# Kernel optimization log

Measured on AMD Instinct MI355X. Metric: run time of the kernel, lower is better.

Reference implementation:

```python
import jax, jax.numpy as jnp
import numpy as np

B, T, V = 512, 200, 2048
E, H, I, A = 20, 100, 64, 32  # embedding, hidden, intermediate, actions


def setup_inputs() -> dict:
    key = jax.random.key(0)
    ks = jax.random.split(key, 12)
    batch = jax.random.uniform(ks[0], (B, T, V), dtype=jnp.float32)
    lengths = jax.random.randint(ks[1], (B,), 1, T + 1)
    s = 0.05
    W_emb = jax.random.normal(ks[2], (E, V), dtype=jnp.float32) * s
    b_emb = jnp.zeros((E,), jnp.float32)
    W_ih = jax.random.normal(ks[3], (4 * H, E), dtype=jnp.float32) * s
    W_hh = jax.random.normal(ks[4], (4 * H, H), dtype=jnp.float32) * s
    b_ih = jnp.zeros((4 * H,), jnp.float32)
    # torch init sets forget-gate bias (second quarter) to 1.0 in bias_hh
    b_hh = jnp.zeros((4 * H,), jnp.float32).at[H:2 * H].set(1.0)
    W1 = jax.random.normal(ks[5], (I, H), dtype=jnp.float32) * s
    b1 = jnp.zeros((I,), jnp.float32)
    W2 = jax.random.normal(ks[6], (A, I), dtype=jnp.float32) * s
    b2 = jnp.zeros((A,), jnp.float32)
    h0 = jnp.zeros((B, H), jnp.float32)
    c0 = jnp.zeros((B, H), jnp.float32)
    return {"batch": batch, "lengths": lengths, "W_emb": W_emb, "b_emb": b_emb,
            "W_ih": W_ih, "W_hh": W_hh, "b_ih": b_ih, "b_hh": b_hh,
            "W1": W1, "b1": b1, "W2": W2, "b2": b2, "h0": h0, "c0": c0}


def reference(batch, lengths, W_emb, b_emb, W_ih, W_hh, b_ih, b_hh,
              W1, b1, W2, b2, h0, c0):
    # Embedding via Linear: [B,T,V] @ [V,E] -> [B,T,E]
    emb = jnp.einsum('btv,ev->bte', batch, W_emb) + b_emb
    # Precompute input contribution to all gates: [B,T,4H]
    xg = jnp.einsum('bte,ge->btg', emb, W_ih) + b_ih + b_hh

    def step(carry, xg_t):
        h, c = carry
        gates = xg_t + h @ W_hh.T  # [B,4H]
        i, f, g, o = jnp.split(gates, 4, axis=-1)  # torch gate order i,f,g,o
        c = jax.nn.sigmoid(f) * c + jax.nn.sigmoid(i) * jnp.tanh(g)
        h = jax.nn.sigmoid(o) * jnp.tanh(c)
        return (h, c), h

    _, ys = jax.lax.scan(step, (h0, c0), jnp.swapaxes(xg, 0, 1))  # ys: [T,B,H]
    nb = batch.shape[0]
    h_final = ys[lengths - 1, jnp.arange(nb)]  # [B,H] output at last valid step
    inter = jax.nn.relu(h_final @ W1.T + b1)
    actions = inter @ W2.T + b2
    return actions
```

## Files before the change

### kernel.cpp

```cpp
#include <hip/hip_runtime.h>

#define BB 512
#define TT 200
#define VV 2048
#define EE 20
#define HH 100
#define G4 400
#define II 64
#define AA 32

typedef _Float16 half8 __attribute__((ext_vector_type(8)));
typedef float    f32x4 __attribute__((ext_vector_type(4)));
typedef float    vf2   __attribute__((ext_vector_type(2)));

#define NCHUNK 64
#define WS_BF_OFF  1024
#define WS_EMB_OFF (1024 + 32768)

__global__ __launch_bounds__(512) void k0_prep(
    const int* __restrict__ lengths, const float* __restrict__ W_emb,
    int* __restrict__ off, _Float16* __restrict__ Bfrag)
{
    if (blockIdx.x == 0) {
        __shared__ int s[BB];
        int tid = threadIdx.x;
        s[tid] = lengths[tid];
        __syncthreads();
        for (int d = 1; d < BB; d <<= 1) {
            int v = (tid >= d) ? s[tid - d] : 0;
            __syncthreads();
            if (tid >= d) s[tid] += v;
            __syncthreads();
        }
        off[tid + 1] = s[tid];
        if (tid == 0) off[0] = 0;
    } else {
        int F = (blockIdx.x - 1) * 512 + threadIdx.x;
        if (F < NCHUNK * 2 * 64 * 8) {
            int e = F & 7, l = (F >> 3) & 63, n = (F >> 9) & 1, c = F >> 10;
            int k = c * 32 + (l >> 4) * 8 + e;
            int col = n * 16 + (l & 15);
            float v = (col < EE) ? W_emb[(size_t)col * VV + k] : 0.f;
            Bfrag[F] = (_Float16)v;
        }
    }
}

__global__ __launch_bounds__(256) void k1_embed(
    const float* __restrict__ batch, const int* __restrict__ off,
    const _Float16* __restrict__ Bfrag, const float* __restrict__ b_emb,
    float* __restrict__ emb)
{
    const int Nv = off[BB];
    if (blockIdx.x * 64 >= Nv) return;

    const int lane  = threadIdx.x & 63;
    const int wid   = threadIdx.x >> 6;
    const int rbase = blockIdx.x * 64 + wid * 16;

    int lrow = rbase + (lane & 15);
    int lr = (lrow < Nv) ? lrow : (Nv - 1);
    int lo = 0, hi = BB;
    while (lo + 1 < hi) {
        int mid = (lo + hi) >> 1;
        if (off[mid] <= lr) lo = mid; else hi = mid;
    }
    const int lroff = lo * TT + (lr - off[lo]);

    const float* __restrict__ aptr = batch + (size_t)lroff * VV + ((lane >> 4) * 8);
    const half8* __restrict__ bptr = reinterpret_cast<const half8*>(Bfrag) + lane;

    f32x4 acc0 = {0.f, 0.f, 0.f, 0.f};
    f32x4 acc1 = {0.f, 0.f, 0.f, 0.f};

#pragma unroll 4
    for (int c = 0; c < NCHUNK; ++c) {
        float4 a0 = *reinterpret_cast<const float4*>(aptr + c * 32);
        float4 a1 = *reinterpret_cast<const float4*>(aptr + c * 32 + 4);
        half8 b0 = bptr[(c * 2 + 0) * 64];
        half8 b1 = bptr[(c * 2 + 1) * 64];
        half8 av;
        av[0] = (_Float16)a0.x; av[1] = (_Float16)a0.y;
        av[2] = (_Float16)a0.z; av[3] = (_Float16)a0.w;
        av[4] = (_Float16)a1.x; av[5] = (_Float16)a1.y;
        av[6] = (_Float16)a1.z; av[7] = (_Float16)a1.w;
        acc0 = __builtin_amdgcn_mfma_f32_16x16x32_f16(av, b0, acc0, 0, 0, 0);
        acc1 = __builtin_amdgcn_mfma_f32_16x16x32_f16(av, b1, acc1, 0, 0, 0);
    }

    const int col0 = lane & 15;
    const float bias0 = b_emb[col0];
    const float bias1 = (col0 < 4) ? b_emb[16 + col0] : 0.f;
#pragma unroll
    for (int r = 0; r < 4; ++r) {
        int s = (lane >> 4) * 4 + r;
        int srow = rbase + s;
        int sroff = __shfl(lroff, s, 64);
        if (srow < Nv) {
            emb[(size_t)sroff * EE + col0] = acc0[r] + bias0;
            if (col0 < 4)
                emb[(size_t)sroff * EE + 16 + col0] = acc1[r] + bias1;
        }
    }
}

__device__ __forceinline__ float fast_sig(float x) { return 1.f / (1.f + __expf(-x)); }
__device__ __forceinline__ float fast_tanh(float x) {
    x = fminf(fmaxf(x, -15.f), 15.f);
    float e = __expf(2.f * x);
    return (e - 1.f) / (e + 1.f);
}
__device__ __forceinline__ float dpp_xor1_add(float v) {
    int p = __builtin_amdgcn_update_dpp(0, __builtin_bit_cast(int, v), 0xB1, 0xF, 0xF, true);
    return v + __builtin_bit_cast(float, p);
}
__device__ __forceinline__ float dpp_xor2_add(float v) {
    int p = __builtin_amdgcn_update_dpp(0, __builtin_bit_cast(int, v), 0x4E, 0xF, 0xF, true);
    return v + __builtin_bit_cast(float, p);
}
#define QSTR 36

__global__ __launch_bounds__(448) void k2_lstm(
    const float* __restrict__ emb, const int* __restrict__ lengths,
    const float* __restrict__ W_ih, const float* __restrict__ W_hh,
    const float* __restrict__ b_ih, const float* __restrict__ b_hh,
    const float* __restrict__ W1, const float* __restrict__ b1,
    const float* __restrict__ W2, const float* __restrict__ b2,
    const float* __restrict__ h0, const float* __restrict__ c0,
    float* __restrict__ out)
{
    __shared__ float emb_lds[2][TT][EE];
    __shared__ float xhbuf[2][2][160];
    __shared__ float hfin[2][HH];
    __shared__ float inter[2][II];

    const int tid = threadIdx.x;
    const int b0  = blockIdx.x * 2;
    const int len0 = lengths[b0];
    const int len1 = lengths[b0 + 1];
    const int tmax = (len0 > len1) ? len0 : len1;

    const int j = tid >> 2, q = tid & 3;

    {
        const float4* srcp = reinterpret_cast<const float4*>(emb + (size_t)b0 * TT * EE);
        float4* dst = reinterpret_cast<float4*>(&emb_lds[0][0][0]);
        for (int i = tid; i < 2 * TT * EE / 4; i += 448) dst[i] = srcp[i];
    }
    for (int i = tid; i < 2 * 2 * 160; i += 448) (&xhbuf[0][0][0])[i] = 0.f;

    vf2 w2[4][16];
    float biasv[4];
    float c_reg = 0.f;
    int lenq = 0;
    if (tid < G4) {
        const int rr[4] = { j, HH + j, 2 * HH + j, 3 * HH + j };
#pragma unroll
        for (int g = 0; g < 4; ++g) {
            const int r = rr[g];
#pragma unroll
            for (int mp = 0; mp < 16; ++mp) {
                int k = q * 32 + mp * 2;
                float2 v;
                if (k + 1 < EE)           v = *reinterpret_cast<const float2*>(&W_ih[r * EE + k]);
                else if (k + 1 < EE + HH) v = *reinterpret_cast<const float2*>(&W_hh[r * HH + k - EE]);
                else                      v = make_float2(0.f, 0.f);
                w2[g][mp].x = v.x; w2[g][mp].y = v.y;
            }
            biasv[g] = b_ih[r] + b_hh[r];
        }
        if (q < 2) c_reg = c0[(size_t)(b0 + q) * HH + j];
        lenq = (q == 0) ? len0 : len1;
    }
    __syncthreads();

    if (tid < G4) {
        if (q < 2) {
            int i = EE + j;
            xhbuf[0][q][(i >> 5) * QSTR + (i & 31)] = h0[(size_t)(b0 + q) * HH + j];
        }
    } else if (tid < G4 + 2 * EE) {
        const int wdx = tid - G4, bw = wdx / EE, e = wdx - bw * EE;
        xhbuf[0][bw][e] = emb_lds[bw][0][e];
    }
    __syncthreads();

#pragma unroll 1
    for (int t = 0; t < tmax; ++t) {
        const int cur = t & 1, nxt = cur ^ 1;
        if (tid < G4) {
            vf2 a[4][2];
#pragma unroll
            for (int g = 0; g < 4; ++g) { a[g][0].x=0.f; a[g][0].y=0.f; a[g][1].x=0.f; a[g][1].y=0.f; }
            const float* xc = &xhbuf[cur][0][0];
#pragma unroll
            for (int m8 = 0; m8 < 8; ++m8) {
                float4 x0 = *reinterpret_cast<const float4*>(xc + q * QSTR + m8 * 4);
                float4 x1 = *reinterpret_cast<const float4*>(xc + 160 + q * QSTR + m8 * 4);
                vf2 xl0, xh0, xl1, xh1;
                xl0.x = x0.x; xl0.y = x0.y;  xh0.x = x0.z; xh0.y = x0.w;
                xl1.x = x1.x; xl1.y = x1.y;  xh1.x = x1.z; xh1.y = x1.w;
#pragma unroll
                for (int g = 0; g < 4; ++g) {
                    a[g][0] = __builtin_elementwise_fma(w2[g][2*m8],   xl0, a[g][0]);
                    a[g][0] = __builtin_elementwise_fma(w2[g][2*m8+1], xh0, a[g][0]);
                    a[g][1] = __builtin_elementwise_fma(w2[g][2*m8],   xl1, a[g][1]);
                    a[g][1] = __builtin_elementwise_fma(w2[g][2*m8+1], xh1, a[g][1]);
                }
            }
            float s_[4][2];
#pragma unroll
            for (int g = 0; g < 4; ++g) {
#pragma unroll
                for (int bb = 0; bb < 2; ++bb) {
                    float v = a[g][bb].x + a[g][bb].y;
                    v = dpp_xor1_add(v);
                    v = dpp_xor2_add(v);
                    s_[g][bb] = v;
                }
            }
            if (q < 2) {
                float gi = s_[0][q] + biasv[0];
                float gf = s_[1][q] + biasv[1];
                float gg = s_[2][q] + biasv[2];
                float go = s_[3][q] + biasv[3];
                c_reg = fast_sig(gf) * c_reg + fast_sig(gi) * fast_tanh(gg);
                float hv = fast_sig(go) * fast_tanh(c_reg);
                int ii = EE + j;
                xhbuf[nxt][q][(ii >> 5) * QSTR + (ii & 31)] = hv;
                if (t == lenq - 1) hfin[q][j] = hv;
            }
        } else if (tid < G4 + 2 * EE) {
            const int wdx = tid - G4, bw = wdx / EE, e = wdx - bw * EE;
            if (t + 1 < TT) xhbuf[nxt][bw][e] = emb_lds[bw][t + 1][e];
        }
        __syncthreads();
    }

    if (tid < 2 * II) {
        int bb = tid >> 6, i = tid & 63;
        float a = b1[i];
        const float* w1r = W1 + i * HH;
#pragma unroll
        for (int k = 0; k < HH; k += 4) {
            a += w1r[k] * hfin[bb][k] + w1r[k+1] * hfin[bb][k+1]
               + w1r[k+2] * hfin[bb][k+2] + w1r[k+3] * hfin[bb][k+3];
        }
        inter[bb][i] = fmaxf(a, 0.f);
    }
    __syncthreads();
    if (tid < 2 * AA) {
        int bb = tid >> 5, ai = tid & 31;
        float a = b2[ai];
        const float* w2r = W2 + ai * II;
#pragma unroll
        for (int k = 0; k < II; ++k) a += w2r[k] * inter[bb][k];
        out[(size_t)(b0 + bb) * AA + ai] = a;
    }
}

extern "C" void kernel_launch(void* const* d_in, const int* in_sizes, int n_in,
                              void* d_out, int out_size, void* d_ws, size_t ws_size,
                              hipStream_t stream) {
    const float* batch  = (const float*)d_in[0];
    const int*   lengths= (const int*)  d_in[1];
    const float* W_emb  = (const float*)d_in[2];
    const float* b_emb  = (const float*)d_in[3];
    const float* W_ih   = (const float*)d_in[4];
    const float* W_hh   = (const float*)d_in[5];
    const float* b_ih   = (const float*)d_in[6];
    const float* b_hh   = (const float*)d_in[7];
    const float* W1     = (const float*)d_in[8];
    const float* b1     = (const float*)d_in[9];
    const float* W2     = (const float*)d_in[10];
    const float* b2     = (const float*)d_in[11];
    const float* h0     = (const float*)d_in[12];
    const float* c0     = (const float*)d_in[13];
    float* out = (float*)d_out;

    int*       off   = (int*)d_ws;
    _Float16*  Bfrag = (_Float16*)((float*)d_ws + WS_BF_OFF);
    float*     emb   = (float*)d_ws + WS_EMB_OFF;

    k0_prep<<<1 + (NCHUNK * 2 * 64 * 8 + 511) / 512, 512, 0, stream>>>(lengths, W_emb, off, Bfrag);
    k1_embed<<<(BB * TT + 63) / 64, 256, 0, stream>>>(batch, off, Bfrag, b_emb, emb);
    k2_lstm<<<BB / 2, 448, 0, stream>>>(emb, lengths, W_ih, W_hh, b_ih, b_hh,
                                        W1, b1, W2, b2, h0, c0, out);
}
```

Before: 401.5 us.

## Process one sequence per LSTM block with packed fp16 weights and mixed FMA

```diff
diff --git a/kernel.cpp b/kernel.cpp
--- a/kernel.cpp
+++ b/kernel.cpp
@@ -11,7 +11,6 @@
 
 typedef _Float16 half8 __attribute__((ext_vector_type(8)));
 typedef float    f32x4 __attribute__((ext_vector_type(4)));
-typedef float    vf2   __attribute__((ext_vector_type(2)));
 
 #define NCHUNK 64
 #define WS_BF_OFF  1024
@@ -105,11 +104,6 @@
 }
 
 __device__ __forceinline__ float fast_sig(float x) { return 1.f / (1.f + __expf(-x)); }
-__device__ __forceinline__ float fast_tanh(float x) {
-    x = fminf(fmaxf(x, -15.f), 15.f);
-    float e = __expf(2.f * x);
-    return (e - 1.f) / (e + 1.f);
-}
 __device__ __forceinline__ float dpp_xor1_add(float v) {
     int p = __builtin_amdgcn_update_dpp(0, __builtin_bit_cast(int, v), 0xB1, 0xF, 0xF, true);
     return v + __builtin_bit_cast(float, p);
@@ -118,9 +112,27 @@
     int p = __builtin_amdgcn_update_dpp(0, __builtin_bit_cast(int, v), 0x4E, 0xF, 0xF, true);
     return v + __builtin_bit_cast(float, p);
 }
+template<int CTRL>
+__device__ __forceinline__ float dpp_mov(float v) {
+    int p = __builtin_amdgcn_update_dpp(0, __builtin_bit_cast(int, v), CTRL, 0xF, 0xF, true);
+    return __builtin_bit_cast(float, p);
+}
+__device__ __forceinline__ void fma_mix_lo(float& acc, unsigned int w, float x) {
+    asm("v_fma_mix_f32 %0, %1, %2, %0 op_sel_hi:[1,0,0]"
+        : "+v"(acc) : "v"(w), "v"(x));
+}
+__device__ __forceinline__ void fma_mix_hi(float& acc, unsigned int w, float x) {
+    asm("v_fma_mix_f32 %0, %1, %2, %0 op_sel:[1,0,0] op_sel_hi:[1,0,0]"
+        : "+v"(acc) : "v"(w), "v"(x));
+}
+__device__ __forceinline__ unsigned int packw(float f0, float f1) {
+    unsigned short u0 = __builtin_bit_cast(unsigned short, (_Float16)f0);
+    unsigned short u1 = __builtin_bit_cast(unsigned short, (_Float16)f1);
+    return ((unsigned int)u1 << 16) | u0;
+}
 #define QSTR 36
 
-__global__ __launch_bounds__(448) void k2_lstm(
+__global__ __launch_bounds__(448, 4) void k2_lstm(
     const float* __restrict__ emb, const int* __restrict__ lengths,
     const float* __restrict__ W_ih, const float* __restrict__ W_hh,
     const float* __restrict__ b_ih, const float* __restrict__ b_hh,
@@ -129,133 +141,124 @@
     const float* __restrict__ h0, const float* __restrict__ c0,
     float* __restrict__ out)
 {
-    __shared__ float emb_lds[2][TT][EE];
-    __shared__ float xhbuf[2][2][160];
-    __shared__ float hfin[2][HH];
-    __shared__ float inter[2][II];
+    __shared__ float emb_lds[TT][EE];
+    __shared__ float xh[2][160];
+    __shared__ float hfin[HH];
+    __shared__ float inter[II];
 
     const int tid = threadIdx.x;
-    const int b0  = blockIdx.x * 2;
-    const int len0 = lengths[b0];
-    const int len1 = lengths[b0 + 1];
-    const int tmax = (len0 > len1) ? len0 : len1;
+    const int b   = blockIdx.x;
+    const int len = lengths[b];
 
     const int j = tid >> 2, q = tid & 3;
 
     {
-        const float4* srcp = reinterpret_cast<const float4*>(emb + (size_t)b0 * TT * EE);
-        float4* dst = reinterpret_cast<float4*>(&emb_lds[0][0][0]);
-        for (int i = tid; i < 2 * TT * EE / 4; i += 448) dst[i] = srcp[i];
-    }
-    for (int i = tid; i < 2 * 2 * 160; i += 448) (&xhbuf[0][0][0])[i] = 0.f;
-
-    vf2 w2[4][16];
+        const float4* srcp = reinterpret_cast<const float4*>(emb + (size_t)b * TT * EE);
+        float4* dst = reinterpret_cast<float4*>(&emb_lds[0][0]);
+        for (int i = tid; i < TT * EE / 4; i += 448) dst[i] = srcp[i];
+    }
+    for (int i = tid; i < 2 * 160; i += 448) (&xh[0][0])[i] = 0.f;
+
+    unsigned int w[4][16];
     float biasv[4];
     float c_reg = 0.f;
-    int lenq = 0;
     if (tid < G4) {
-        const int rr[4] = { j, HH + j, 2 * HH + j, 3 * HH + j };
 #pragma unroll
         for (int g = 0; g < 4; ++g) {
-            const int r = rr[g];
-#pragma unroll
-            for (int mp = 0; mp < 16; ++mp) {
-                int k = q * 32 + mp * 2;
-                float2 v;
-                if (k + 1 < EE)           v = *reinterpret_cast<const float2*>(&W_ih[r * EE + k]);
-                else if (k + 1 < EE + HH) v = *reinterpret_cast<const float2*>(&W_hh[r * HH + k - EE]);
-                else                      v = make_float2(0.f, 0.f);
-                w2[g][mp].x = v.x; w2[g][mp].y = v.y;
+            const int r = g * HH + j;
+#pragma unroll
+            for (int p = 0; p < 16; ++p) {
+                int s0 = q * 32 + 2 * p;
+                float f0 = (s0 < EE) ? W_ih[r * EE + s0]
+                         : (s0 < EE + HH) ? W_hh[r * HH + s0 - EE] : 0.f;
+                int s1 = s0 + 1;
+                float f1 = (s1 < EE) ? W_ih[r * EE + s1]
+                         : (s1 < EE + HH) ? W_hh[r * HH + s1 - EE] : 0.f;
+                w[g][p] = packw(f0, f1);
             }
             biasv[g] = b_ih[r] + b_hh[r];
         }
-        if (q < 2) c_reg = c0[(size_t)(b0 + q) * HH + j];
-        lenq = (q == 0) ? len0 : len1;
+        if (q == 0) c_reg = c0[(size_t)b * HH + j];
     }
     __syncthreads();
 
     if (tid < G4) {
-        if (q < 2) {
-            int i = EE + j;
-            xhbuf[0][q][(i >> 5) * QSTR + (i & 31)] = h0[(size_t)(b0 + q) * HH + j];
-        }
-    } else if (tid < G4 + 2 * EE) {
-        const int wdx = tid - G4, bw = wdx / EE, e = wdx - bw * EE;
-        xhbuf[0][bw][e] = emb_lds[bw][0][e];
+        if (q == 0) {
+            int s = EE + j;
+            xh[0][(s >> 5) * QSTR + (s & 31)] = h0[(size_t)b * HH + j];
+        }
+    } else if (tid < G4 + EE) {
+        const int e = tid - G4;
+        xh[0][e] = emb_lds[0][e];
     }
     __syncthreads();
 
 #pragma unroll 1
-    for (int t = 0; t < tmax; ++t) {
+    for (int t = 0; t < len; ++t) {
         const int cur = t & 1, nxt = cur ^ 1;
         if (tid < G4) {
-            vf2 a[4][2];
-#pragma unroll
-            for (int g = 0; g < 4; ++g) { a[g][0].x=0.f; a[g][0].y=0.f; a[g][1].x=0.f; a[g][1].y=0.f; }
-            const float* xc = &xhbuf[cur][0][0];
-#pragma unroll
-            for (int m8 = 0; m8 < 8; ++m8) {
-                float4 x0 = *reinterpret_cast<const float4*>(xc + q * QSTR + m8 * 4);
-                float4 x1 = *reinterpret_cast<const float4*>(xc + 160 + q * QSTR + m8 * 4);
-                vf2 xl0, xh0, xl1, xh1;
-                xl0.x = x0.x; xl0.y = x0.y;  xh0.x = x0.z; xh0.y = x0.w;
-                xl1.x = x1.x; xl1.y = x1.y;  xh1.x = x1.z; xh1.y = x1.w;
+            float acc[4][2];
+#pragma unroll
+            for (int g = 0; g < 4; ++g) { acc[g][0] = 0.f; acc[g][1] = 0.f; }
+            const float* xc = &xh[cur][q * QSTR];
+#pragma unroll
+            for (int m = 0; m < 8; ++m) {
+                float4 xv = *reinterpret_cast<const float4*>(xc + 4 * m);
 #pragma unroll
                 for (int g = 0; g < 4; ++g) {
-                    a[g][0] = __builtin_elementwise_fma(w2[g][2*m8],   xl0, a[g][0]);
-                    a[g][0] = __builtin_elementwise_fma(w2[g][2*m8+1], xh0, a[g][0]);
-                    a[g][1] = __builtin_elementwise_fma(w2[g][2*m8],   xl1, a[g][1]);
-                    a[g][1] = __builtin_elementwise_fma(w2[g][2*m8+1], xh1, a[g][1]);
+                    fma_mix_lo(acc[g][0], w[g][2 * m],     xv.x);
+                    fma_mix_hi(acc[g][1], w[g][2 * m],     xv.y);
+                    fma_mix_lo(acc[g][0], w[g][2 * m + 1], xv.z);
+                    fma_mix_hi(acc[g][1], w[g][2 * m + 1], xv.w);
                 }
             }
-            float s_[4][2];
+            float s_[4];
 #pragma unroll
             for (int g = 0; g < 4; ++g) {
-#pragma unroll
-                for (int bb = 0; bb < 2; ++bb) {
-                    float v = a[g][bb].x + a[g][bb].y;
-                    v = dpp_xor1_add(v);
-                    v = dpp_xor2_add(v);
-                    s_[g][bb] = v;
-                }
-            }
-            if (q < 2) {
-                float gi = s_[0][q] + biasv[0];
-                float gf = s_[1][q] + biasv[1];
-                float gg = s_[2][q] + biasv[2];
-                float go = s_[3][q] + biasv[3];
-                c_reg = fast_sig(gf) * c_reg + fast_sig(gi) * fast_tanh(gg);
-                float hv = fast_sig(go) * fast_tanh(c_reg);
-                int ii = EE + j;
-                xhbuf[nxt][q][(ii >> 5) * QSTR + (ii & 31)] = hv;
-                if (t == lenq - 1) hfin[q][j] = hv;
-            }
-        } else if (tid < G4 + 2 * EE) {
-            const int wdx = tid - G4, bw = wdx / EE, e = wdx - bw * EE;
-            if (t + 1 < TT) xhbuf[nxt][bw][e] = emb_lds[bw][t + 1][e];
+                float v = acc[g][0] + acc[g][1];
+                v = dpp_xor1_add(v);
+                v = dpp_xor2_add(v);
+                s_[g] = v + biasv[g];
+            }
+            float sq = (q == 0) ? s_[0] : (q == 1) ? s_[1] : (q == 2) ? s_[2] : s_[3];
+            float aa = (q == 2) ? 2.f : 1.f;
+            float u  = fast_sig(aa * sq);
+            float nq = u * aa - (aa - 1.f);
+            float nf = dpp_mov<0xB1>(nq);
+            float ng = dpp_mov<0x4E>(nq);
+            float no = dpp_mov<0x1B>(nq);
+            if (q == 0) {
+                c_reg = nf * c_reg + nq * ng;
+                float tc = 2.f * fast_sig(2.f * c_reg) - 1.f;
+                float hv = no * tc;
+                const int s = EE + j;
+                xh[nxt][(s >> 5) * QSTR + (s & 31)] = hv;
+                if (t == len - 1) hfin[j] = hv;
+            }
+        } else if (tid < G4 + EE) {
+            const int e = tid - G4;
+            if (t + 1 < TT) xh[nxt][e] = emb_lds[t + 1][e];
         }
         __syncthreads();
     }
 
-    if (tid < 2 * II) {
-        int bb = tid >> 6, i = tid & 63;
-        float a = b1[i];
-        const float* w1r = W1 + i * HH;
+    if (tid < II) {
+        float a = b1[tid];
+        const float* w1r = W1 + tid * HH;
 #pragma unroll
         for (int k = 0; k < HH; k += 4) {
-            a += w1r[k] * hfin[bb][k] + w1r[k+1] * hfin[bb][k+1]
-               + w1r[k+2] * hfin[bb][k+2] + w1r[k+3] * hfin[bb][k+3];
-        }
-        inter[bb][i] = fmaxf(a, 0.f);
+            a += w1r[k] * hfin[k] + w1r[k + 1] * hfin[k + 1]
+               + w1r[k + 2] * hfin[k + 2] + w1r[k + 3] * hfin[k + 3];
+        }
+        inter[tid] = fmaxf(a, 0.f);
     }
     __syncthreads();
-    if (tid < 2 * AA) {
-        int bb = tid >> 5, ai = tid & 31;
-        float a = b2[ai];
-        const float* w2r = W2 + ai * II;
-#pragma unroll
-        for (int k = 0; k < II; ++k) a += w2r[k] * inter[bb][k];
-        out[(size_t)(b0 + bb) * AA + ai] = a;
+    if (tid < AA) {
+        float a = b2[tid];
+        const float* w2r = W2 + tid * II;
+#pragma unroll
+        for (int k = 0; k < II; ++k) a += w2r[k] * inter[k];
+        out[(size_t)b * AA + tid] = a;
     }
 }
 
@@ -284,6 +287,6 @@
 
     k0_prep<<<1 + (NCHUNK * 2 * 64 * 8 + 511) / 512, 512, 0, stream>>>(lengths, W_emb, off, Bfrag);
     k1_embed<<<(BB * TT + 63) / 64, 256, 0, stream>>>(batch, off, Bfrag, b_emb, emb);
-    k2_lstm<<<BB / 2, 448, 0, stream>>>(emb, lengths, W_ih, W_hh, b_ih, b_hh,
-                                        W1, b1, W2, b2, h0, c0, out);
-}
+    k2_lstm<<<BB, 448, 0, stream>>>(emb, lengths, W_ih, W_hh, b_ih, b_hh,
+                                    W1, b1, W2, b2, h0, c0, out);
+}
```

New measurement: 453.8 us. +13.0%, slower.

## Precompute input gates with MFMA and run LSTM recurrence via fp16 MFMA over 16 sequences

Applied to the files above, without the earlier changes.

```diff
diff --git a/kernel.cpp b/kernel.cpp
--- a/kernel.cpp
+++ b/kernel.cpp
@@ -8,18 +8,26 @@
 #define G4 400
 #define II 64
 #define AA 32
+#define NT 25
+#define NCHUNK 64
 
 typedef _Float16 half8 __attribute__((ext_vector_type(8)));
 typedef float    f32x4 __attribute__((ext_vector_type(4)));
-typedef float    vf2   __attribute__((ext_vector_type(2)));
-
-#define NCHUNK 64
-#define WS_BF_OFF  1024
-#define WS_EMB_OFF (1024 + 32768)
+
+#define WS_BF_OFF    1024
+#define WS_WIHF_OFF  (WS_BF_OFF + 32768)
+#define WS_WHHF_OFF  (WS_WIHF_OFF + 6400)
+#define WS_BIASC_OFF (WS_WHHF_OFF + 25600)
+#define WS_EMB_OFF   (WS_BIASC_OFF + 400)
+#define WS_XG_OFF    (WS_EMB_OFF + 2048000)
 
 __global__ __launch_bounds__(512) void k0_prep(
     const int* __restrict__ lengths, const float* __restrict__ W_emb,
-    int* __restrict__ off, _Float16* __restrict__ Bfrag)
+    const float* __restrict__ W_ih, const float* __restrict__ W_hh,
+    const float* __restrict__ b_ih, const float* __restrict__ b_hh,
+    int* __restrict__ off, _Float16* __restrict__ Bfrag,
+    _Float16* __restrict__ Wihf, _Float16* __restrict__ Whhf,
+    float* __restrict__ biasc)
 {
     if (blockIdx.x == 0) {
         __shared__ int s[BB];
@@ -34,15 +42,41 @@
         }
         off[tid + 1] = s[tid];
         if (tid == 0) off[0] = 0;
-    } else {
-        int F = (blockIdx.x - 1) * 512 + threadIdx.x;
-        if (F < NCHUNK * 2 * 64 * 8) {
-            int e = F & 7, l = (F >> 3) & 63, n = (F >> 9) & 1, c = F >> 10;
-            int k = c * 32 + (l >> 4) * 8 + e;
-            int col = n * 16 + (l & 15);
-            float v = (col < EE) ? W_emb[(size_t)col * VV + k] : 0.f;
-            Bfrag[F] = (_Float16)v;
-        }
+        return;
+    }
+    int F = (blockIdx.x - 1) * 512 + threadIdx.x;
+    if (F < 65536) {
+        int e = F & 7, l = (F >> 3) & 63, nn = (F >> 9) & 1, c = F >> 10;
+        int k = c * 32 + (l >> 4) * 8 + e;
+        int col = nn * 16 + (l & 15);
+        float v = (col < EE) ? W_emb[(size_t)col * VV + k] : 0.f;
+        Bfrag[F] = (_Float16)v;
+        return;
+    }
+    F -= 65536;
+    if (F < 12800) {
+        int e = F & 7, l = (F >> 3) & 63, nt = F >> 9;
+        int rp = nt * 16 + (l & 15);
+        int j = rp >> 2, g = rp & 3;
+        int k = 8 * (l >> 4) + e;
+        float v = (k < EE) ? W_ih[(size_t)(g * HH + j) * EE + k] : 0.f;
+        Wihf[F] = (_Float16)v;
+        return;
+    }
+    F -= 12800;
+    if (F < 51200) {
+        int e = F & 7, l = (F >> 3) & 63, c = (F >> 9) & 3, m = F >> 11;
+        int rp = m * 16 + (l & 15);
+        int j = rp >> 2, g = rp & 3;
+        int k = 32 * c + 8 * (l >> 4) + e;
+        float v = (k < HH) ? W_hh[(size_t)(g * HH + j) * HH + k] : 0.f;
+        Whhf[F] = (_Float16)v;
+        return;
+    }
+    F -= 51200;
+    if (F < 400) {
+        int j = F >> 2, g = F & 3;
+        biasc[F] = b_ih[g * HH + j] + b_hh[g * HH + j];
     }
 }
 
@@ -93,169 +127,176 @@
     const float bias1 = (col0 < 4) ? b_emb[16 + col0] : 0.f;
 #pragma unroll
     for (int r = 0; r < 4; ++r) {
-        int s = (lane >> 4) * 4 + r;
-        int srow = rbase + s;
-        int sroff = __shfl(lroff, s, 64);
+        int srow = rbase + (lane >> 4) * 4 + r;
         if (srow < Nv) {
-            emb[(size_t)sroff * EE + col0] = acc0[r] + bias0;
+            emb[(size_t)srow * EE + col0] = acc0[r] + bias0;
             if (col0 < 4)
-                emb[(size_t)sroff * EE + 16 + col0] = acc1[r] + bias1;
+                emb[(size_t)srow * EE + 16 + col0] = acc1[r] + bias1;
         }
     }
 }
 
+__global__ __launch_bounds__(256, 2) void k1_xg(
+    const float* __restrict__ emb, const int* __restrict__ off,
+    const _Float16* __restrict__ Wihf, const float* __restrict__ biasc,
+    float* __restrict__ xg)
+{
+    __shared__ __align__(16) uint4 wl[NT * 64];
+    __shared__ float bl[G4];
+
+    const int tid = threadIdx.x;
+    const int Nv = off[BB];
+    for (int i = tid; i < NT * 64; i += 256) wl[i] = reinterpret_cast<const uint4*>(Wihf)[i];
+    for (int i = tid; i < G4; i += 256) bl[i] = biasc[i];
+    __syncthreads();
+
+    const int lane = tid & 63, wid = tid >> 6;
+    const int T = blockIdx.x * 4 + wid;
+    if (T * 16 >= Nv) return;
+
+    const int lr = min(T * 16 + (lane & 15), Nv - 1);
+    const int kb = (lane >> 4) * 8;
+    const float* ap = emb + (size_t)lr * EE;
+    float4 p0 = make_float4(0.f, 0.f, 0.f, 0.f), p1 = p0;
+    if (kb < EE)     p0 = *reinterpret_cast<const float4*>(ap + kb);
+    if (kb + 4 < EE) p1 = *reinterpret_cast<const float4*>(ap + kb + 4);
+    half8 av;
+    av[0] = (_Float16)p0.x; av[1] = (_Float16)p0.y;
+    av[2] = (_Float16)p0.z; av[3] = (_Float16)p0.w;
+    av[4] = (_Float16)p1.x; av[5] = (_Float16)p1.y;
+    av[6] = (_Float16)p1.z; av[7] = (_Float16)p1.w;
+
+    const int rbase = T * 16 + 4 * (lane >> 4);
+    const int cl = lane & 15;
+#pragma unroll
+    for (int nt = 0; nt < NT; ++nt) {
+        half8 bf = *reinterpret_cast<const half8*>(&wl[nt * 64 + lane]);
+        f32x4 a = {0.f, 0.f, 0.f, 0.f};
+        a = __builtin_amdgcn_mfma_f32_16x16x32_f16(av, bf, a, 0, 0, 0);
+        float bias = bl[nt * 16 + cl];
+#pragma unroll
+        for (int r = 0; r < 4; ++r) {
+            if (rbase + r < Nv)
+                xg[(size_t)(rbase + r) * G4 + nt * 16 + cl] = a[r] + bias;
+        }
+    }
+}
+
 __device__ __forceinline__ float fast_sig(float x) { return 1.f / (1.f + __expf(-x)); }
-__device__ __forceinline__ float fast_tanh(float x) {
-    x = fminf(fmaxf(x, -15.f), 15.f);
-    float e = __expf(2.f * x);
-    return (e - 1.f) / (e + 1.f);
-}
-__device__ __forceinline__ float dpp_xor1_add(float v) {
-    int p = __builtin_amdgcn_update_dpp(0, __builtin_bit_cast(int, v), 0xB1, 0xF, 0xF, true);
-    return v + __builtin_bit_cast(float, p);
-}
-__device__ __forceinline__ float dpp_xor2_add(float v) {
-    int p = __builtin_amdgcn_update_dpp(0, __builtin_bit_cast(int, v), 0x4E, 0xF, 0xF, true);
-    return v + __builtin_bit_cast(float, p);
-}
-#define QSTR 36
-
-__global__ __launch_bounds__(448) void k2_lstm(
-    const float* __restrict__ emb, const int* __restrict__ lengths,
-    const float* __restrict__ W_ih, const float* __restrict__ W_hh,
-    const float* __restrict__ b_ih, const float* __restrict__ b_hh,
+__device__ __forceinline__ float fast_tanh(float x) { return 2.f * fast_sig(2.f * x) - 1.f; }
+
+#define STEP(T_, CUR_, XC_, XN_)  do {                                                        \
+    uint4 rb0_ = *reinterpret_cast<const uint4*>(&bfrag[CUR_][0][lane][0]);                   \
+    uint4 rb1_ = *reinterpret_cast<const uint4*>(&bfrag[CUR_][1][lane][0]);                   \
+    uint4 rb2_ = *reinterpret_cast<const uint4*>(&bfrag[CUR_][2][lane][0]);                   \
+    uint4 rb3_ = *reinterpret_cast<const uint4*>(&bfrag[CUR_][3][lane][0]);                   \
+    _Pragma("unroll")                                                                         \
+    for (int it = 0; it < 4; ++it) if (it < ntile)                                            \
+        XN_[it] = *reinterpret_cast<const float4*>(xg + rowbase + (size_t)((T_) + 1) * G4 + xgoff[it]); \
+    _Pragma("unroll")                                                                         \
+    for (int it = 0; it < 4; ++it) if (it < ntile) {                                          \
+        f32x4 acc = __builtin_bit_cast(f32x4, XC_[it]);                                       \
+        acc = __builtin_amdgcn_mfma_f32_16x16x32_f16(af[it][0], __builtin_bit_cast(half8, rb0_), acc, 0, 0, 0); \
+        acc = __builtin_amdgcn_mfma_f32_16x16x32_f16(af[it][1], __builtin_bit_cast(half8, rb1_), acc, 0, 0, 0); \
+        acc = __builtin_amdgcn_mfma_f32_16x16x32_f16(af[it][2], __builtin_bit_cast(half8, rb2_), acc, 0, 0, 0); \
+        acc = __builtin_amdgcn_mfma_f32_16x16x32_f16(af[it][3], __builtin_bit_cast(half8, rb3_), acc, 0, 0, 0); \
+        float gi = fast_sig(acc[0]);                                                          \
+        float gf = fast_sig(acc[1]);                                                          \
+        float gg = fast_tanh(acc[2]);                                                         \
+        float go = fast_sig(acc[3]);                                                          \
+        cst[it] = gf * cst[it] + gi * gg;                                                     \
+        float hv = go * fast_tanh(cst[it]);                                                   \
+        int j_ = jidx[it];                                                                    \
+        if ((T_) == len_n - 1) hfin[n][j_] = hv;                                              \
+        int kk_ = j_ & 31;                                                                    \
+        _Float16* hp_ = (_Float16*)&bfrag[(CUR_) ^ 1][j_ >> 5][((kk_ >> 3) << 4) | n][(kk_ & 7) >> 1]; \
+        hp_[kk_ & 1] = (_Float16)hv;                                                          \
+    }                                                                                         \
+    __syncthreads();                                                                          \
+} while (0)
+
+__global__ __launch_bounds__(512, 2) void k2_lstm(
+    const float* __restrict__ xg, const int* __restrict__ lengths,
+    const int* __restrict__ off, const _Float16* __restrict__ Whhf,
     const float* __restrict__ W1, const float* __restrict__ b1,
     const float* __restrict__ W2, const float* __restrict__ b2,
     const float* __restrict__ h0, const float* __restrict__ c0,
     float* __restrict__ out)
 {
-    __shared__ float emb_lds[2][TT][EE];
-    __shared__ float xhbuf[2][2][160];
-    __shared__ float hfin[2][HH];
-    __shared__ float inter[2][II];
-
-    const int tid = threadIdx.x;
-    const int b0  = blockIdx.x * 2;
-    const int len0 = lengths[b0];
-    const int len1 = lengths[b0 + 1];
-    const int tmax = (len0 > len1) ? len0 : len1;
-
-    const int j = tid >> 2, q = tid & 3;
-
-    {
-        const float4* srcp = reinterpret_cast<const float4*>(emb + (size_t)b0 * TT * EE);
-        float4* dst = reinterpret_cast<float4*>(&emb_lds[0][0][0]);
-        for (int i = tid; i < 2 * TT * EE / 4; i += 448) dst[i] = srcp[i];
-    }
-    for (int i = tid; i < 2 * 2 * 160; i += 448) (&xhbuf[0][0][0])[i] = 0.f;
-
-    vf2 w2[4][16];
-    float biasv[4];
-    float c_reg = 0.f;
-    int lenq = 0;
-    if (tid < G4) {
-        const int rr[4] = { j, HH + j, 2 * HH + j, 3 * HH + j };
-#pragma unroll
-        for (int g = 0; g < 4; ++g) {
-            const int r = rr[g];
-#pragma unroll
-            for (int mp = 0; mp < 16; ++mp) {
-                int k = q * 32 + mp * 2;
-                float2 v;
-                if (k + 1 < EE)           v = *reinterpret_cast<const float2*>(&W_ih[r * EE + k]);
-                else if (k + 1 < EE + HH) v = *reinterpret_cast<const float2*>(&W_hh[r * HH + k - EE]);
-                else                      v = make_float2(0.f, 0.f);
-                w2[g][mp].x = v.x; w2[g][mp].y = v.y;
-            }
-            biasv[g] = b_ih[r] + b_hh[r];
-        }
-        if (q < 2) c_reg = c0[(size_t)(b0 + q) * HH + j];
-        lenq = (q == 0) ? len0 : len1;
-    }
+    __shared__ __align__(16) unsigned int bfrag[2][4][64][4];
+    __shared__ float hfin[16][HH];
+    __shared__ float inter[16][II];
+    __shared__ int len_s[16], off_s[16];
+
+    const int tid  = threadIdx.x;
+    const int lane = tid & 63;
+    const int w    = tid >> 6;
+    const int b0   = blockIdx.x * 16;
+    const int n    = lane & 15, rg = lane >> 4;
+
+    if (tid < 16) {
+        len_s[tid] = lengths[b0 + tid];
+        off_s[tid] = off[b0 + tid];
+    }
+    for (int i = tid; i < 2 * 4 * 64 * 4; i += 512) (&bfrag[0][0][0][0])[i] = 0u;
     __syncthreads();
 
-    if (tid < G4) {
-        if (q < 2) {
-            int i = EE + j;
-            xhbuf[0][q][(i >> 5) * QSTR + (i & 31)] = h0[(size_t)(b0 + q) * HH + j];
-        }
-    } else if (tid < G4 + 2 * EE) {
-        const int wdx = tid - G4, bw = wdx / EE, e = wdx - bw * EE;
-        xhbuf[0][bw][e] = emb_lds[bw][0][e];
+    int tmax = 0;
+#pragma unroll
+    for (int k = 0; k < 16; ++k) tmax = max(tmax, len_s[k]);
+
+    const int ntile = (w == 7) ? 4 : 3;
+    const int m0    = (w < 7) ? 3 * w : 21;
+    const int len_n = len_s[n];
+    const size_t rowbase = (size_t)off_s[n] * G4;
+
+    half8 af[4][4];
+    float cst[4];
+    int   jidx[4], xgoff[4];
+    float4 xgA[4], xgB[4];
+#pragma unroll
+    for (int it = 0; it < 4; ++it) if (it < ntile) {
+        const int m = m0 + it;
+#pragma unroll
+        for (int c = 0; c < 4; ++c)
+            af[it][c] = reinterpret_cast<const half8*>(Whhf)[((m * 4 + c) * 64) + lane];
+        const int j = 4 * m + rg;
+        jidx[it]  = j;
+        xgoff[it] = 16 * m + 4 * rg;
+        cst[it] = c0[(size_t)(b0 + n) * HH + j];
+        float hv = h0[(size_t)(b0 + n) * HH + j];
+        int kk = j & 31;
+        _Float16* hp = (_Float16*)&bfrag[0][j >> 5][((kk >> 3) << 4) | n][(kk & 7) >> 1];
+        hp[kk & 1] = (_Float16)hv;
+        xgA[it] = *reinterpret_cast<const float4*>(xg + rowbase + xgoff[it]);
     }
     __syncthreads();
 
-#pragma unroll 1
-    for (int t = 0; t < tmax; ++t) {
-        const int cur = t & 1, nxt = cur ^ 1;
-        if (tid < G4) {
-            vf2 a[4][2];
-#pragma unroll
-            for (int g = 0; g < 4; ++g) { a[g][0].x=0.f; a[g][0].y=0.f; a[g][1].x=0.f; a[g][1].y=0.f; }
-            const float* xc = &xhbuf[cur][0][0];
-#pragma unroll
-            for (int m8 = 0; m8 < 8; ++m8) {
-                float4 x0 = *reinterpret_cast<const float4*>(xc + q * QSTR + m8 * 4);
-                float4 x1 = *reinterpret_cast<const float4*>(xc + 160 + q * QSTR + m8 * 4);
-                vf2 xl0, xh0, xl1, xh1;
-                xl0.x = x0.x; xl0.y = x0.y;  xh0.x = x0.z; xh0.y = x0.w;
-                xl1.x = x1.x; xl1.y = x1.y;  xh1.x = x1.z; xh1.y = x1.w;
-#pragma unroll
-                for (int g = 0; g < 4; ++g) {
-                    a[g][0] = __builtin_elementwise_fma(w2[g][2*m8],   xl0, a[g][0]);
-                    a[g][0] = __builtin_elementwise_fma(w2[g][2*m8+1], xh0, a[g][0]);
-                    a[g][1] = __builtin_elementwise_fma(w2[g][2*m8],   xl1, a[g][1]);
-                    a[g][1] = __builtin_elementwise_fma(w2[g][2*m8+1], xh1, a[g][1]);
-                }
-            }
-            float s_[4][2];
-#pragma unroll
-            for (int g = 0; g < 4; ++g) {
-#pragma unroll
-                for (int bb = 0; bb < 2; ++bb) {
-                    float v = a[g][bb].x + a[g][bb].y;
-                    v = dpp_xor1_add(v);
-                    v = dpp_xor2_add(v);
-                    s_[g][bb] = v;
-                }
-            }
-            if (q < 2) {
-                float gi = s_[0][q] + biasv[0];
-                float gf = s_[1][q] + biasv[1];
-                float gg = s_[2][q] + biasv[2];
-                float go = s_[3][q] + biasv[3];
-                c_reg = fast_sig(gf) * c_reg + fast_sig(gi) * fast_tanh(gg);
-                float hv = fast_sig(go) * fast_tanh(c_reg);
-                int ii = EE + j;
-                xhbuf[nxt][q][(ii >> 5) * QSTR + (ii & 31)] = hv;
-                if (t == lenq - 1) hfin[q][j] = hv;
-            }
-        } else if (tid < G4 + 2 * EE) {
-            const int wdx = tid - G4, bw = wdx / EE, e = wdx - bw * EE;
-            if (t + 1 < TT) xhbuf[nxt][bw][e] = emb_lds[bw][t + 1][e];
-        }
-        __syncthreads();
-    }
-
-    if (tid < 2 * II) {
-        int bb = tid >> 6, i = tid & 63;
+    for (int t = 0; t < tmax; t += 2) {
+        STEP(t, 0, xgA, xgB);
+        if (t + 1 < tmax) STEP(t + 1, 1, xgB, xgA);
+    }
+
+    for (int o = tid; o < 16 * II; o += 512) {
+        int nn = o >> 6, i = o & 63;
         float a = b1[i];
         const float* w1r = W1 + i * HH;
+        const float* hr  = &hfin[nn][0];
 #pragma unroll
         for (int k = 0; k < HH; k += 4) {
-            a += w1r[k] * hfin[bb][k] + w1r[k+1] * hfin[bb][k+1]
-               + w1r[k+2] * hfin[bb][k+2] + w1r[k+3] * hfin[bb][k+3];
+            a += w1r[k] * hr[k] + w1r[k + 1] * hr[k + 1]
+               + w1r[k + 2] * hr[k + 2] + w1r[k + 3] * hr[k + 3];
         }
-        inter[bb][i] = fmaxf(a, 0.f);
+        inter[nn][i] = fmaxf(a, 0.f);
     }
     __syncthreads();
-    if (tid < 2 * AA) {
-        int bb = tid >> 5, ai = tid & 31;
+    for (int o = tid; o < 16 * AA; o += 512) {
+        int nn = o >> 5, ai = o & 31;
         float a = b2[ai];
         const float* w2r = W2 + ai * II;
 #pragma unroll
-        for (int k = 0; k < II; ++k) a += w2r[k] * inter[bb][k];
-        out[(size_t)(b0 + bb) * AA + ai] = a;
+        for (int k = 0; k < II; ++k) a += w2r[k] * inter[nn][k];
+        out[(size_t)(b0 + nn) * AA + ai] = a;
     }
 }
 
@@ -279,11 +320,18 @@
     float* out = (float*)d_out;
 
     int*       off   = (int*)d_ws;
-    _Float16*  Bfrag = (_Float16*)((float*)d_ws + WS_BF_OFF);
-    float*     emb   = (float*)d_ws + WS_EMB_OFF;
-
-    k0_prep<<<1 + (NCHUNK * 2 * 64 * 8 + 511) / 512, 512, 0, stream>>>(lengths, W_emb, off, Bfrag);
+    float*     wsf   = (float*)d_ws;
+    _Float16*  Bfrag = (_Float16*)(wsf + WS_BF_OFF);
+    _Float16*  Wihf  = (_Float16*)(wsf + WS_WIHF_OFF);
+    _Float16*  Whhf  = (_Float16*)(wsf + WS_WHHF_OFF);
+    float*     biasc = wsf + WS_BIASC_OFF;
+    float*     emb   = wsf + WS_EMB_OFF;
+    float*     xg    = wsf + WS_XG_OFF;
+
+    k0_prep<<<255, 512, 0, stream>>>(lengths, W_emb, W_ih, W_hh, b_ih, b_hh,
+                                     off, Bfrag, Wihf, Whhf, biasc);
     k1_embed<<<(BB * TT + 63) / 64, 256, 0, stream>>>(batch, off, Bfrag, b_emb, emb);
-    k2_lstm<<<BB / 2, 448, 0, stream>>>(emb, lengths, W_ih, W_hh, b_ih, b_hh,
-                                        W1, b1, W2, b2, h0, c0, out);
-}
+    k1_xg<<<(BB * TT / 16 + 3) / 4, 256, 0, stream>>>(emb, off, Wihf, biasc, xg);
+    k2_lstm<<<BB / 16, 512, 0, stream>>>(xg, lengths, off, Whhf,
+                                         W1, b1, W2, b2, h0, c0, out);
+}
```

Result: slower. 432.4 us (+7.7%).
